# Performance work log

Measured on AMD Instinct MI355X. Metric: run time of the kernel, lower is better.

## Reference

```python
import jax, jax.numpy as jnp
import numpy as np

B, N, HID = 2, 512, 768
BIAF = 256
CLS = 14
CH = 32
SIZE_DIM = 25
N_POS = 30
HSZ = 2 * (BIAF + 1) + SIZE_DIM


def setup_inputs() -> dict:
    key = jax.random.key(0)
    ks = jax.random.split(key, 16)
    s = 0.02
    return {
        "x": jax.random.normal(ks[0], (B, N, HID), jnp.float32),
        "y": jax.random.normal(ks[1], (B, N, HID), jnp.float32),
        "z": jax.random.normal(ks[2], (B, N, N, CH), jnp.float32),
        "mlp1_w": jax.random.normal(ks[3], (BIAF, HID), jnp.float32) * s,
        "mlp1_b": jnp.zeros((BIAF,), jnp.float32),
        "mlp2_w": jax.random.normal(ks[4], (BIAF, HID), jnp.float32) * s,
        "mlp2_b": jnp.zeros((BIAF,), jnp.float32),
        "head_w": jax.random.normal(ks[5], (BIAF, HID), jnp.float32) * s,
        "head_b": jnp.zeros((BIAF,), jnp.float32),
        "tail_w": jax.random.normal(ks[6], (BIAF, HID), jnp.float32) * s,
        "tail_b": jnp.zeros((BIAF,), jnp.float32),
        "biaf_W": jax.random.normal(ks[7], (CLS, BIAF + 1, BIAF + 1), jnp.float32) * s,
        "W": jax.random.normal(ks[8], (CLS, HSZ), jnp.float32) * s,
        "size_emb": jax.random.normal(ks[9], (N_POS, SIZE_DIM), jnp.float32) * s,
    }


def reference(x, y, z, mlp1_w, mlp1_b, mlp2_w, mlp2_b, head_w, head_b,
              tail_w, tail_b, biaf_W, W, size_emb):
    # MLP branches (dropout=0 at eval; torch GELU is exact erf)
    h = jax.nn.gelu(x @ mlp1_w.T + mlp1_b, approximate=False)   # (b,m,BIAF)
    t = jax.nn.gelu(y @ mlp2_w.T + mlp2_b, approximate=False)   # (b,n,BIAF)
    ones = jnp.ones(h.shape[:-1] + (1,), h.dtype)
    h1 = jnp.concatenate([h, ones], -1)                          # (b,m,BIAF+1)
    t1 = jnp.concatenate([t, ones], -1)                          # (b,n,BIAF+1)
    # Biaffine with bias_x=bias_y=True -> (b,cls,m,n)
    o1 = jnp.einsum('bmi,kij,bnj->bkmn', h1, biaf_W, t1)

    # head/tail MLPs with LeakyReLU(0.01), then append 1-column
    head = jax.nn.leaky_relu(x @ head_w.T + head_b, 0.01)
    tail = jax.nn.leaky_relu(x @ tail_w.T + tail_b, 0.01)
    head = jnp.concatenate([head, ones], -1)                     # (b,m,BIAF+1)
    tail = jnp.concatenate([tail, ones], -1)                     # (b,n,BIAF+1)

    # einsum('bmnh,kh->bkmn', cat([head_m, tail_n, size_mn]), W) decomposed so
    # the (b,m,n,HSZ) pairwise tensor is never materialized (same math).
    d = head.shape[-1]
    Wh, Wt, Ws = W[:, :d], W[:, d:2 * d], W[:, 2 * d:]
    n = x.shape[1]
    ar = jnp.arange(n)
    ids = jnp.clip(ar[None, :] - ar[:, None], -N_POS // 2, N_POS // 2 - 1) + N_POS // 2
    se = size_emb[ids]                                           # (m,n,SIZE_DIM)
    o3 = (jnp.einsum('bmh,kh->bkm', head, Wh)[:, :, :, None]
          + jnp.einsum('bnh,kh->bkn', tail, Wt)[:, :, None, :]
          + jnp.einsum('mnh,kh->kmn', se, Ws)[None])
    return o1 + o3
```

## Files before the change

kernel.cpp:

```cpp
#include <hip/hip_runtime.h>
#include <hip/hip_bf16.h>
#include <math.h>
#include <stdint.h>

#define BDIM 2
#define NDIM 512
#define HID 768
#define BIAF 256
#define CLS 14
#define DD 257
#define NPOS 30
#define SDIM 25
#define HSZ 539
#define PK 288
#define PJ 384

typedef unsigned short ushort_t;
typedef __attribute__((ext_vector_type(8))) short short8;
typedef __attribute__((ext_vector_type(4))) float floatx4;
typedef __attribute__((ext_vector_type(4))) unsigned short ushort4_t;

#define MFMA16(a, b, c) __builtin_amdgcn_mfma_f32_16x16x32_bf16((a), (b), (c), 0, 0, 0)

__device__ inline float bf2f(ushort_t u) {
    union { unsigned int i; float f; } c; c.i = ((unsigned)u) << 16; return c.f;
}
__device__ inline ushort_t f2bf(float f) {
    __hip_bfloat16 h = __float2bfloat16(f);
    return *(ushort_t*)&h;
}

__device__ inline int xcd_swz(int bid, int nwg) {
    int q = nwg >> 3;
    return (bid & 7) * q + (bid >> 3);
}

__device__ inline void glds16(const ushort_t* g, const ushort_t* l) {
    __builtin_amdgcn_global_load_lds(
        (const __attribute__((address_space(1))) unsigned int*)(unsigned long long)(uintptr_t)g,
        (__attribute__((address_space(3))) unsigned int*)(unsigned int)(uintptr_t)l,
        16, 0, 0);
}


__global__ __launch_bounds__(256) void prep_proj(
    const float* __restrict__ x, const float* __restrict__ y,
    const float* __restrict__ m1w, const float* __restrict__ m2w,
    const float* __restrict__ hw,  const float* __restrict__ tw,
    const float* __restrict__ m1b, const float* __restrict__ m2b,
    const float* __restrict__ hb,  const float* __restrict__ tb,
    const float* __restrict__ biafW, ushort_t* __restrict__ packW,
    ushort_t* __restrict__ h1hi, ushort_t* __restrict__ h1lo,
    ushort_t* __restrict__ t1hi, ushort_t* __restrict__ t1lo,
    float* __restrict__ headf, float* __restrict__ tailf)
{
    __shared__ __align__(16) ushort_t Sh[2 * 4096];
    const int bid = blockIdx.x;
    const int tid = threadIdx.x;

    if (bid >= 2536) {
        int idx = (bid - 2536) * 256 + tid;
        int plane = idx >> 15;
        int tok = (idx >> 5) & 1023;
        int c   = 256 + (idx & 31);
        ushort_t* dst = (plane == 0) ? h1hi : (plane == 1) ? h1lo : (plane == 2) ? t1hi : t1lo;
        ushort_t val = (c == 256 && (plane == 0 || plane == 2)) ? (ushort_t)0x3F80 : (ushort_t)0;
        dst[(size_t)tok * PK + c] = val;
        return;
    }
    if (bid >= 1024) {
        float (*tile)[33] = reinterpret_cast<float(*)[33]>(Sh);
        const int rb = bid - 1024;
        const int ix = rb % 9;
        const int jy = (rb / 9) % 12;
        const int k  = rb / 108;
        const int i0 = ix * 32, j0 = jy * 32;
        const int r8 = tid >> 5;
        const int c  = tid & 31;
        #pragma unroll
        for (int rr = 0; rr < 4; ++rr) {
            int r = rr * 8 + r8;
            int gi = i0 + r, gj = j0 + c;
            tile[r][c] = (gi < DD && gj < DD) ? biafW[((size_t)k * DD + gi) * DD + gj] : 0.f;
        }
        __syncthreads();
        #pragma unroll
        for (int rr = 0; rr < 4; ++rr) {
            int jr = rr * 8 + r8;
            packW[((size_t)k * PJ + (j0 + jr)) * PK + i0 + c] = f2bf(tile[c][jr]);
        }
        return;
    }

    const int flat = xcd_swz(bid, 1024);
    const int ft  = flat & 7;
    const int mt2 = (flat >> 3) & 31;
    const int proj = flat >> 8;
    const int wave = tid >> 6, L = tid & 63;
    const int quad = L >> 4, l16 = L & 15;
    const int mi = wave >> 1, fi = wave & 1;
    const int rbase = (l16 >> 1) * 64 + (((((l16 & 1) << 2) | quad) ^ (l16 >> 1)) * 8);

    const int srw = tid >> 3, sc4 = tid & 7;
    const int sA = srw >> 4, rr = srw & 15;
    const int woffe = ((rr >> 1) * 64)
                    + (((((rr & 1) << 2) | (sc4 >> 1)) ^ ((rr >> 1) & 7)) * 8)
                    + (sc4 & 1) * 4;
    const int segA = sA * 512 + woffe;

    const float* asrc = (proj == 1) ? y : x;
    const float* wsrc = (proj == 0) ? m1w : (proj == 1) ? m2w : (proj == 2) ? hw : tw;
    const float* bias = (proj == 0) ? m1b : (proj == 1) ? m2b : (proj == 2) ? hb : tb;
    const float* aptr = asrc + (size_t)(mt2 * 32 + srw) * HID + sc4 * 4;
    const float* wptr = wsrc + (size_t)(ft * 32 + srw) * HID + sc4 * 4;

    auto cvt_write = [&](int bo, float4 av, float4 wv) {
        ushort_t* B = Sh + bo * 4096;
        float aa[4] = {av.x, av.y, av.z, av.w};
        ushort4_t ah, al;
        #pragma unroll
        for (int j = 0; j < 4; ++j) {
            ushort_t h = f2bf(aa[j]);
            ah[j] = h;
            al[j] = f2bf(aa[j] - bf2f(h));
        }
        *(ushort4_t*)(B + segA) = ah;
        *(ushort4_t*)(B + 1024 + segA) = al;
        float ww[4] = {wv.x, wv.y, wv.z, wv.w};
        ushort4_t wh, wl;
        #pragma unroll
        for (int j = 0; j < 4; ++j) {
            ushort_t h = f2bf(ww[j]);
            wh[j] = h;
            wl[j] = f2bf(ww[j] - bf2f(h));
        }
        *(ushort4_t*)(B + 2048 + segA) = wh;
        *(ushort4_t*)(B + 3072 + segA) = wl;
    };

    floatx4 acc = {0.f, 0.f, 0.f, 0.f};

    float4 pa = *(const float4*)(aptr);
    float4 pw = *(const float4*)(wptr);
    cvt_write(0, pa, pw);
    pa = *(const float4*)(aptr + 32);
    pw = *(const float4*)(wptr + 32);
    __syncthreads();

    int cur = 0;
    #pragma unroll 2
    for (int t = 0; t < 24; ++t) {
        if (t < 23) {
            cvt_write(cur ^ 1, pa, pw);
            if (t < 22) {
                int k2 = (t + 2) * 32;
                pa = *(const float4*)(aptr + k2);
                pw = *(const float4*)(wptr + k2);
            }
        }
        const ushort_t* B = Sh + cur * 4096;
        short8 ah = *(const short8*)(B + mi * 512 + rbase);
        short8 al = *(const short8*)(B + 1024 + mi * 512 + rbase);
        short8 bh = *(const short8*)(B + 2048 + fi * 512 + rbase);
        short8 bl = *(const short8*)(B + 3072 + fi * 512 + rbase);
        acc = MFMA16(ah, bh, acc);
        acc = MFMA16(al, bh, acc);
        acc = MFMA16(ah, bl, acc);
        __syncthreads();
        cur ^= 1;
    }

    {
        int feat = ft * 32 + fi * 16 + l16;
        float bv = bias[feat];
        #pragma unroll
        for (int r = 0; r < 4; ++r) {
            int tok = mt2 * 32 + mi * 16 + quad * 4 + r;
            float v = acc[r] + bv;
            if (proj <= 1) {
                float g = 0.5f * v * (1.0f + erff(v * 0.70710678118654752f));
                ushort_t h = f2bf(g);
                ushort_t lo = f2bf(g - bf2f(h));
                if (proj == 0) { h1hi[(size_t)tok * PK + feat] = h; h1lo[(size_t)tok * PK + feat] = lo; }
                else           { t1hi[(size_t)tok * PK + feat] = h; t1lo[(size_t)tok * PK + feat] = lo; }
            } else {
                float lv = (v >= 0.f) ? v : 0.01f * v;
                if (proj == 2) headf[(size_t)tok * 256 + feat] = lv;
                else           tailf[(size_t)tok * 256 + feat] = lv;
            }
        }
    }
}

__global__ __launch_bounds__(256) void mb_hk(
    const ushort_t* __restrict__ h1hi, const ushort_t* __restrict__ h1lo,
    const ushort_t* __restrict__ packW,
    ushort_t* __restrict__ Ab,
    const float* __restrict__ headf, const float* __restrict__ tailf,
    const float* __restrict__ W, const float* __restrict__ semb,
    float* __restrict__ hk, float* __restrict__ tk, float* __restrict__ skp)
{
    const int bid = blockIdx.x;
    if (bid >= 672) {
        const int hb = bid - 672;
        if (hb >= 128) {
            int idx = (hb - 128) * 256 + threadIdx.x;
            if (idx < CLS * NPOS) {
                int k = idx / NPOS, d = idx % NPOS;
                float acc = 0.f;
                for (int h = 0; h < SDIM; ++h)
                    acc += semb[d*SDIM + h] * W[k*HSZ + 2*DD + h];
                skp[idx] = acc;
            }
            return;
        }
        int p = hb * 256 + threadIdx.x;
        int which = p >> 14;
        int idx = p & 16383;
        int tok = idx >> 4;
        int k = idx & 15;
        if (k >= CLS) return;
        const float* row = (which ? tailf : headf) + (size_t)tok * 256;
        const float* wr = W + (size_t)k * HSZ + (which ? DD : 0);
        float acc = 0.f;
        for (int f4 = 0; f4 < 64; ++f4) {
            float4 rv = *(const float4*)(row + f4 * 4);
            acc += rv.x * wr[f4*4] + rv.y * wr[f4*4+1] + rv.z * wr[f4*4+2] + rv.w * wr[f4*4+3];
        }
        acc += wr[256];
        float* dst = which ? tk : hk;
        dst[(size_t)(tok >> 9) * CLS * NDIM + (size_t)k * NDIM + (tok & 511)] = acc;
        return;
    }

    __shared__ ushort_t Ah[2 * 2048];
    __shared__ ushort_t Al[2 * 2048];
    __shared__ ushort_t Bt[2 * 3072];
    const int flat = xcd_swz(bid, 672);
    const int jt = flat % 3, mt = (flat / 3) % 8, bk = flat / 24;
    const int b = bk / CLS, k = bk % CLS;
    const int tid = threadIdx.x;
    const int wave = tid >> 6, L = tid & 63;
    const int quad = L >> 4, l16 = L & 15;
    const int sr = L >> 3, u = (L & 7) ^ sr;
    const int srow = 2 * sr + (u >> 2);
    const int scol = (u & 3) * 8;
    const int rbase = (l16 >> 1) * 64 + ((((((l16 & 1) << 2) | quad)) ^ (l16 >> 1)) * 8);
    const int m0 = mt * 64, j0 = jt * 96;
    const int wm = (wave >> 1) * 32, wj = (wave & 1) * 48;

    const ushort_t* gAh = h1hi + (size_t)(b * NDIM + m0) * PK;
    const ushort_t* gAl = h1lo + (size_t)(b * NDIM + m0) * PK;
    const ushort_t* gB  = packW + ((size_t)k * PJ + j0) * PK;

    auto stage = [&](int bo, int k0) {
        for (int s = wave; s < 14; s += 4) {
            const ushort_t* g; const ushort_t* l;
            if (s < 4)      { l = Ah + bo * 2048 + s * 512;       g = gAh + (size_t)(s * 16 + srow) * PK + k0 + scol; }
            else if (s < 8) { l = Al + bo * 2048 + (s - 4) * 512; g = gAl + (size_t)((s - 4) * 16 + srow) * PK + k0 + scol; }
            else            { l = Bt + bo * 3072 + (s - 8) * 512; g = gB  + (size_t)((s - 8) * 16 + srow) * PK + k0 + scol; }
            glds16(g, l);
        }
    };

    floatx4 acc[2][3];
    #pragma unroll
    for (int mi = 0; mi < 2; ++mi)
        #pragma unroll
        for (int ni = 0; ni < 3; ++ni)
            #pragma unroll
            for (int r = 0; r < 4; ++r) acc[mi][ni][r] = 0.f;

    stage(0, 0);
    __syncthreads();
    int cur = 0;
    for (int t = 0; t < 9; ++t) {
        if (t < 8) stage(cur ^ 1, (t + 1) * 32);
        short8 ah[2], al[2], bb[3];
        #pragma unroll
        for (int mi = 0; mi < 2; ++mi) {
            ah[mi] = *(const short8*)(Ah + cur * 2048 + (wm + mi * 16) * 32 + rbase);
            al[mi] = *(const short8*)(Al + cur * 2048 + (wm + mi * 16) * 32 + rbase);
        }
        #pragma unroll
        for (int ni = 0; ni < 3; ++ni)
            bb[ni] = *(const short8*)(Bt + cur * 3072 + (wj + ni * 16) * 32 + rbase);
        #pragma unroll
        for (int mi = 0; mi < 2; ++mi)
            #pragma unroll
            for (int ni = 0; ni < 3; ++ni) {
                acc[mi][ni] = MFMA16(ah[mi], bb[ni], acc[mi][ni]);
                acc[mi][ni] = MFMA16(al[mi], bb[ni], acc[mi][ni]);
            }
        __syncthreads();
        cur ^= 1;
    }

    ushort_t* Aout = Ab + (size_t)bk * NDIM * PK;
    #pragma unroll
    for (int mi = 0; mi < 2; ++mi) {
        #pragma unroll
        for (int r = 0; r < 4; ++r) {
            int row = m0 + wm + mi * 16 + quad * 4 + r;
            #pragma unroll
            for (int ni = 0; ni < 3; ++ni) {
                int col = j0 + wj + ni * 16 + l16;
                Aout[(size_t)row * PK + col] = f2bf(acc[mi][ni][r]);
            }
        }
    }
}

__global__ __launch_bounds__(256) void mo_tile(
    const ushort_t* __restrict__ Ab,
    const ushort_t* __restrict__ t1hi, const ushort_t* __restrict__ t1lo,
    const float* __restrict__ hk, const float* __restrict__ tk,
    const float* __restrict__ sk,
    float* __restrict__ out)
{
    __shared__ ushort_t At[2 * 2048];
    __shared__ ushort_t Bh[2 * 4096];
    __shared__ ushort_t Bl[2 * 4096];
    __shared__ float skr[NPOS];
    const int flat = xcd_swz(blockIdx.x, 896);
    const int nt = flat & 3, mt = (flat >> 2) & 7, bk = flat >> 5;
    const int b = bk / CLS, k = bk % CLS;
    const int tid = threadIdx.x;
    if (tid < NPOS) skr[tid] = sk[k * NPOS + tid];
    const int wave = tid >> 6, L = tid & 63;
    const int quad = L >> 4, l16 = L & 15;
    const int sr = L >> 3, u = (L & 7) ^ sr;
    const int srow = 2 * sr + (u >> 2);
    const int scol = (u & 3) * 8;
    const int rbase = (l16 >> 1) * 64 + ((((((l16 & 1) << 2) | quad)) ^ (l16 >> 1)) * 8);
    const int m0 = mt * 64, n0 = nt * 128;
    const int wm = (wave >> 1) * 32, wn = (wave & 1) * 64;

    const ushort_t* gA  = Ab + ((size_t)bk * NDIM + m0) * PK;
    const ushort_t* gBh = t1hi + (size_t)(b * NDIM + n0) * PK;
    const ushort_t* gBl = t1lo + (size_t)(b * NDIM + n0) * PK;

    auto stage = [&](int bo, int k0) {
        for (int s = wave; s < 20; s += 4) {
            const ushort_t* g; const ushort_t* l;
            if (s < 4)       { l = At + bo * 2048 + s * 512;         g = gA  + (size_t)(s * 16 + srow) * PK + k0 + scol; }
            else if (s < 12) { l = Bh + bo * 4096 + (s - 4) * 512;   g = gBh + (size_t)((s - 4) * 16 + srow) * PK + k0 + scol; }
            else             { l = Bl + bo * 4096 + (s - 12) * 512;  g = gBl + (size_t)((s - 12) * 16 + srow) * PK + k0 + scol; }
            glds16(g, l);
        }
    };

    floatx4 acc[2][4];
    #pragma unroll
    for (int mi = 0; mi < 2; ++mi)
        #pragma unroll
        for (int ni = 0; ni < 4; ++ni)
            #pragma unroll
            for (int r = 0; r < 4; ++r) acc[mi][ni][r] = 0.f;

    stage(0, 0);
    __syncthreads();
    int cur = 0;
    for (int t = 0; t < 9; ++t) {
        if (t < 8) stage(cur ^ 1, (t + 1) * 32);
        short8 a[2], bh[4], bl[4];
        #pragma unroll
        for (int mi = 0; mi < 2; ++mi)
            a[mi] = *(const short8*)(At + cur * 2048 + (wm + mi * 16) * 32 + rbase);
        #pragma unroll
        for (int ni = 0; ni < 4; ++ni) {
            bh[ni] = *(const short8*)(Bh + cur * 4096 + (wn + ni * 16) * 32 + rbase);
            bl[ni] = *(const short8*)(Bl + cur * 4096 + (wn + ni * 16) * 32 + rbase);
        }
        #pragma unroll
        for (int mi = 0; mi < 2; ++mi)
            #pragma unroll
            for (int ni = 0; ni < 4; ++ni) {
                acc[mi][ni] = MFMA16(a[mi], bh[ni], acc[mi][ni]);
                acc[mi][ni] = MFMA16(a[mi], bl[ni], acc[mi][ni]);
            }
        __syncthreads();
        cur ^= 1;
    }

    const size_t obase = (size_t)bk * NDIM;
    #pragma unroll
    for (int mi = 0; mi < 2; ++mi) {
        #pragma unroll
        for (int r = 0; r < 4; ++r) {
            int row = m0 + wm + mi * 16 + quad * 4 + r;
            float hv = hk[obase + row];
            #pragma unroll
            for (int ni = 0; ni < 4; ++ni) {
                int col = n0 + wn + ni * 16 + l16;
                int d = col - row; d = d < -15 ? -15 : (d > 14 ? 14 : d); d += 15;
                out[(obase + row) * NDIM + col] = acc[mi][ni][r] + hv + tk[obase + col] + skr[d];
            }
        }
    }
}

extern "C" void kernel_launch(void* const* d_in, const int* in_sizes, int n_in,
                              void* d_out, int out_size, void* d_ws, size_t ws_size,
                              hipStream_t stream) {
    const float* x    = (const float*)d_in[0];
    const float* y    = (const float*)d_in[1];
    const float* m1w  = (const float*)d_in[3];
    const float* m1b  = (const float*)d_in[4];
    const float* m2w  = (const float*)d_in[5];
    const float* m2b  = (const float*)d_in[6];
    const float* hw   = (const float*)d_in[7];
    const float* hb   = (const float*)d_in[8];
    const float* tw   = (const float*)d_in[9];
    const float* tb   = (const float*)d_in[10];
    const float* biafW= (const float*)d_in[11];
    const float* W    = (const float*)d_in[12];
    const float* semb = (const float*)d_in[13];

    char* p = (char*)d_ws;
    float* hk   = (float*)p;                    p += 57344;
    float* tk   = (float*)p;                    p += 57344;
    float* skp  = (float*)p;                    p += 2048;
    float* headf= (float*)p;                    p += 1048576;
    float* tailf= (float*)p;                    p += 1048576;
    ushort_t* h1hi = (ushort_t*)p;              p += 589824;
    ushort_t* h1lo = (ushort_t*)p;              p += 589824;
    ushort_t* t1hi = (ushort_t*)p;              p += 589824;
    ushort_t* t1lo = (ushort_t*)p;              p += 589824;
    ushort_t* packW= (ushort_t*)p;              p += 3096576;
    ushort_t* Abuf = (ushort_t*)p;              p += 8257536;

    prep_proj<<<3048, 256, 0, stream>>>(x, y, m1w, m2w, hw, tw,
                                        m1b, m2b, hb, tb,
                                        biafW, packW,
                                        h1hi, h1lo, t1hi, t1lo, headf, tailf);
    mb_hk<<<802, 256, 0, stream>>>(h1hi, h1lo, packW, Abuf,
                                   headf, tailf, W, semb, hk, tk, skp);
    mo_tile<<<896, 256, 0, stream>>>(Abuf, t1hi, t1lo, hk, tk, skp,
                                     (float*)d_out);
}
```

Before: 176.4 us.

## Deepen global-to-LDS prefetch with explicit vmcnt waits and raw barriers

Both biaffine GEMM kernels now issue the global_load_lds staging for two K-tiles before the loop. Each iteration waits with a partial vmcnt, so only the older tile must have landed and the newer tile's loads stay in flight across the barrier. The projection kernel swaps __syncthreads for a plain lgkmcnt wait plus s_barrier, avoiding a full vmcnt drain behind its register-prefetched global loads. The hand-counted vmcnt values depend on the per-wave number of staged loads, so a wrong count could race, and the extra barrier per iteration adds some sync cost.

```diff
diff --git a/kernel.cpp b/kernel.cpp
--- a/kernel.cpp
+++ b/kernel.cpp
@@ -41,6 +41,7 @@
         (__attribute__((address_space(3))) unsigned int*)(unsigned int)(uintptr_t)l,
         16, 0, 0);
 }
+
 
 
 __global__ __launch_bounds__(256) void prep_proj(
@@ -145,7 +146,7 @@
     cvt_write(0, pa, pw);
     pa = *(const float4*)(aptr + 32);
     pw = *(const float4*)(wptr + 32);
-    __syncthreads();
+    asm volatile("s_waitcnt lgkmcnt(0)\n\ts_barrier" ::: "memory");
 
     int cur = 0;
     #pragma unroll 2
@@ -166,7 +167,7 @@
         acc = MFMA16(ah, bh, acc);
         acc = MFMA16(al, bh, acc);
         acc = MFMA16(ah, bl, acc);
-        __syncthreads();
+        asm volatile("s_waitcnt lgkmcnt(0)\n\ts_barrier" ::: "memory");
         cur ^= 1;
     }
 
@@ -272,10 +273,12 @@
             for (int r = 0; r < 4; ++r) acc[mi][ni][r] = 0.f;
 
     stage(0, 0);
-    __syncthreads();
+    stage(1, 32);
+    if (wave < 2) asm volatile("s_waitcnt vmcnt(4)\n\ts_barrier" ::: "memory");
+    else          asm volatile("s_waitcnt vmcnt(3)\n\ts_barrier" ::: "memory");
+
     int cur = 0;
     for (int t = 0; t < 9; ++t) {
-        if (t < 8) stage(cur ^ 1, (t + 1) * 32);
         short8 ah[2], al[2], bb[3];
         #pragma unroll
         for (int mi = 0; mi < 2; ++mi) {
@@ -292,7 +295,15 @@
                 acc[mi][ni] = MFMA16(ah[mi], bb[ni], acc[mi][ni]);
                 acc[mi][ni] = MFMA16(al[mi], bb[ni], acc[mi][ni]);
             }
-        __syncthreads();
+        if (t == 8) break;
+        asm volatile("s_barrier" ::: "memory");
+        if (t < 7) {
+            stage(cur, (t + 2) * 32);
+            if (wave < 2) asm volatile("s_waitcnt vmcnt(4)\n\ts_barrier" ::: "memory");
+            else          asm volatile("s_waitcnt vmcnt(3)\n\ts_barrier" ::: "memory");
+        } else {
+            asm volatile("s_waitcnt vmcnt(0)\n\ts_barrier" ::: "memory");
+        }
         cur ^= 1;
     }
 
@@ -359,10 +370,11 @@
             for (int r = 0; r < 4; ++r) acc[mi][ni][r] = 0.f;
 
     stage(0, 0);
-    __syncthreads();
+    stage(1, 32);
+    asm volatile("s_waitcnt vmcnt(5)\n\ts_barrier" ::: "memory");
+
     int cur = 0;
     for (int t = 0; t < 9; ++t) {
-        if (t < 8) stage(cur ^ 1, (t + 1) * 32);
         short8 a[2], bh[4], bl[4];
         #pragma unroll
         for (int mi = 0; mi < 2; ++mi)
@@ -379,7 +391,14 @@
                 acc[mi][ni] = MFMA16(a[mi], bh[ni], acc[mi][ni]);
                 acc[mi][ni] = MFMA16(a[mi], bl[ni], acc[mi][ni]);
             }
-        __syncthreads();
+        if (t == 8) break;
+        asm volatile("s_barrier" ::: "memory");
+        if (t < 7) {
+            stage(cur, (t + 2) * 32);
+            asm volatile("s_waitcnt vmcnt(5)\n\ts_barrier" ::: "memory");
+        } else {
+            asm volatile("s_waitcnt vmcnt(0)\n\ts_barrier" ::: "memory");
+        }
         cur ^= 1;
     }
 
```

After: 175.4 us. No clear change (-0.6%).
